# Kernel optimization log

Hardware: AMD Instinct MI355X
Metric: run time of the kernel (lower is better)

Reference implementation:

```python
import jax, jax.numpy as jnp
import numpy as np

D_MODEL = 2048
N_HEADS = 16
HEAD_DIM = D_MODEL // N_HEADS
LN_EPS = 1e-6  # flax.linen.LayerNorm default
NEG_INF = float('-inf')


def _layernorm_scale_only(x, scale):
    # flax LayerNorm with use_bias=False: normalize over last axis, scale only
    mean = jnp.mean(x, axis=-1, keepdims=True)
    var = jnp.var(x, axis=-1, keepdims=True)
    return (x - mean) * jax.lax.rsqrt(var + LN_EPS) * scale


def setup_inputs() -> dict:
    key = jax.random.key(0)
    ks = jax.random.split(key, 4)
    B, S = 2, 2048
    x = jax.random.normal(ks[0], (B, S, D_MODEL), dtype=jnp.float32)
    Wqkv = jax.random.normal(ks[1], (D_MODEL, 3 * D_MODEL), dtype=jnp.float32) * 0.02
    q_ln_scale = jnp.ones((D_MODEL,), dtype=jnp.float32)
    k_ln_scale = jnp.ones((D_MODEL,), dtype=jnp.float32)
    out_W = jax.random.normal(ks[2], (D_MODEL, D_MODEL), dtype=jnp.float32) * 0.02
    return {"x": x, "Wqkv": Wqkv, "q_ln_scale": q_ln_scale,
            "k_ln_scale": k_ln_scale, "out_W": out_W}


def reference(x, Wqkv, q_ln_scale, k_ln_scale, out_W):
    B, S, _ = x.shape
    qkv = jnp.einsum('bsd,de->bse', x, Wqkv)  # [B,S,3*D] (no bias)
    q, k, v = jnp.split(qkv, 3, axis=-1)
    # QK LayerNorm (attn_qk_ln=True, no bias)
    q = _layernorm_scale_only(q, q_ln_scale)
    k = _layernorm_scale_only(k, k_ln_scale)
    # split heads: [B,S,H,Dh]
    q = q.reshape(B, S, N_HEADS, HEAD_DIM)
    k = k.reshape(B, S, N_HEADS, HEAD_DIM)
    v = v.reshape(B, S, N_HEADS, HEAD_DIM)
    # scaled scores [B,H,S,S]
    scores = jnp.einsum('bshd,bthd->bhst', q / jnp.sqrt(jnp.float32(HEAD_DIM)), k)
    # causal mask: triu(ones, k=1) marks strictly-future positions -> -inf
    causal = jnp.triu(jnp.ones((S, S), dtype=bool), 1)
    scores = jnp.where(causal, NEG_INF, scores)
    # kv-cache mask: arange(S) < S - past_position - S = 0 -> all False (no-op
    # with past_position=0 and no layer_past), faithfully omitted.
    attn = jax.nn.softmax(scores, axis=-1)
    ctx = jnp.einsum('bhst,bthd->bshd', attn, v)  # [B,S,H,Dh]
    out = jnp.einsum('bsd,de->bse', ctx.reshape(B, S, D_MODEL), out_W)
    return out
```

## Files before the change

### kernel.cpp

```cpp
#include <hip/hip_runtime.h>


typedef float f32x4 __attribute__((ext_vector_type(4)));
typedef short s16x8 __attribute__((ext_vector_type(8)));
typedef short s16x4 __attribute__((ext_vector_type(4)));

static __device__ __forceinline__ unsigned short f2bf(float f) {
  unsigned u = __builtin_bit_cast(unsigned, f);
  unsigned r = u + 0x7fffu + ((u >> 16) & 1u);
  return (unsigned short)(r >> 16);
}
static __device__ __forceinline__ float bf2f(unsigned short s) {
  unsigned u = ((unsigned)s) << 16;
  return __builtin_bit_cast(float, u);
}

static __device__ __forceinline__ void gload_lds16(const unsigned short* g, unsigned short* l) {
  __builtin_amdgcn_global_load_lds((const __attribute__((address_space(1))) void*)g,
                                   (__attribute__((address_space(3))) void*)l, 16, 0, 0);
}

__global__ __launch_bounds__(256) void k_cvt4(const float4* __restrict__ in,
                                              s16x4* __restrict__ out, int n) {
  int i = blockIdx.x * 256 + threadIdx.x;
  if (i >= n) return;
  float4 v = in[i];
  s16x4 o = { (short)f2bf(v.x), (short)f2bf(v.y), (short)f2bf(v.z), (short)f2bf(v.w) };
  out[i] = o;
}

__global__ __launch_bounds__(256) void k_twT(const float* __restrict__ in,
                                             unsigned short* __restrict__ out,
                                             int K, int N) {
  __shared__ float tile[32][33];
  const int n0 = blockIdx.x * 32, k0 = blockIdx.y * 32;
  const int tx = threadIdx.x & 31, ty = threadIdx.x >> 5;
#pragma unroll
  for (int rr = 0; rr < 4; ++rr) {
    int kr = ty + rr * 8;
    tile[kr][tx] = in[(size_t)(k0 + kr) * N + n0 + tx];
  }
  __syncthreads();
#pragma unroll
  for (int rr = 0; rr < 4; ++rr) {
    int nr = ty + rr * 8;
    out[(size_t)(n0 + nr) * K + k0 + tx] = f2bf(tile[tx][nr]);
  }
}

template <int BF16OUT>
__global__ __launch_bounds__(512, 2) void k_g8p(const unsigned short* __restrict__ A,
                                                const unsigned short* __restrict__ Bt,
                                                void* __restrict__ Cout,
                                                int N, int K, int nbn) {
  __shared__ unsigned short sA[2 * 128 * 64];
  __shared__ unsigned short sB[2 * 2 * 128 * 64];
  const int t = threadIdx.x;
  const int wid = t >> 6, lane = t & 63, g = lane >> 4, l15 = lane & 15;
  const int wm2 = wid >> 2, wn2 = wid & 3;
  const int xr = l15 & 7;

  const int cpx = (int)gridDim.x >> 3;
  const int swz = ((int)blockIdx.x & 7) * cpx + ((int)blockIdx.x >> 3);
  const int m0 = (swz / nbn) * 128, n0 = (swz % nbn) * 256;

  const int srow = t >> 3;
  const int sslot = (t & 7) ^ (srow & 7);
  const unsigned short* pA = A  + (size_t)(m0 + srow) * K + sslot * 8;
  const unsigned short* pB = Bt + (size_t)(n0 + srow) * K + sslot * 8;

  auto stageA = [&](int kt) {
#pragma unroll
    for (int j = 0; j < 2; ++j)
      gload_lds16(pA + (size_t)(j * 64) * K + kt * 64,
                  sA + (kt & 1) * 8192 + j * 4096 + t * 8);
  };
  auto stageB = [&](int kt, int h) {
#pragma unroll
    for (int j = 0; j < 2; ++j)
      gload_lds16(pB + (size_t)(h * 128 + j * 64) * K + kt * 64,
                  sB + (kt & 1) * 16384 + h * 8192 + j * 4096 + t * 8);
  };

  const int sl0 = (g ^ xr) * 8, sl1 = ((4 + g) ^ xr) * 8;
  const int arow = wm2 * 64 + l15;
  const int brow = wn2 * 32 + l15;

  f32x4 acc[2][4][2];
#pragma unroll
  for (int h = 0; h < 2; ++h)
#pragma unroll
    for (int fm = 0; fm < 4; ++fm)
#pragma unroll
      for (int fn = 0; fn < 2; ++fn) acc[h][fm][fn] = (f32x4){0.f, 0.f, 0.f, 0.f};

  const int NK = K >> 6;
  stageA(0); stageB(0, 0); stageB(0, 1);
  asm volatile("s_waitcnt vmcnt(2)" ::: "memory");
  __builtin_amdgcn_sched_barrier(0);
  asm volatile("s_barrier" ::: "memory");

  for (int s = 0; s < NK; ++s) {
    const unsigned short* aT = sA + (s & 1) * 8192;
    const unsigned short* bT = sB + (s & 1) * 16384;
    const bool tail = (s == NK - 1);
    s16x8 af[4][2], bfr[2][2];

#pragma unroll
    for (int fm = 0; fm < 4; ++fm) {
      af[fm][0] = *(const s16x8*)&aT[(arow + fm * 16) * 64 + sl0];
      af[fm][1] = *(const s16x8*)&aT[(arow + fm * 16) * 64 + sl1];
    }
#pragma unroll
    for (int fn = 0; fn < 2; ++fn) {
      bfr[fn][0] = *(const s16x8*)&bT[(brow + fn * 16) * 64 + sl0];
      bfr[fn][1] = *(const s16x8*)&bT[(brow + fn * 16) * 64 + sl1];
    }
    if (!tail) { stageA(s + 1); stageB(s + 1, 0); }
    if (tail) asm volatile("s_waitcnt vmcnt(0)" ::: "memory");
    else      asm volatile("s_waitcnt vmcnt(4)" ::: "memory");
    __builtin_amdgcn_sched_barrier(0);
    asm volatile("s_barrier" ::: "memory");
    __builtin_amdgcn_s_setprio(1);
#pragma unroll
    for (int fm = 0; fm < 4; ++fm)
#pragma unroll
      for (int fn = 0; fn < 2; ++fn)
#pragma unroll
        for (int ks = 0; ks < 2; ++ks)
          acc[0][fm][fn] = __builtin_amdgcn_mfma_f32_16x16x32_bf16(
              af[fm][ks], bfr[fn][ks], acc[0][fm][fn], 0, 0, 0);
    __builtin_amdgcn_s_setprio(0);
    asm volatile("s_barrier" ::: "memory");

#pragma unroll
    for (int fn = 0; fn < 2; ++fn) {
      bfr[fn][0] = *(const s16x8*)&bT[8192 + (brow + fn * 16) * 64 + sl0];
      bfr[fn][1] = *(const s16x8*)&bT[8192 + (brow + fn * 16) * 64 + sl1];
    }
    if (!tail) stageB(s + 1, 1);
    if (tail) asm volatile("s_waitcnt vmcnt(0)" ::: "memory");
    else      asm volatile("s_waitcnt vmcnt(2)" ::: "memory");
    __builtin_amdgcn_sched_barrier(0);
    asm volatile("s_barrier" ::: "memory");
    __builtin_amdgcn_s_setprio(1);
#pragma unroll
    for (int fm = 0; fm < 4; ++fm)
#pragma unroll
      for (int fn = 0; fn < 2; ++fn)
#pragma unroll
        for (int ks = 0; ks < 2; ++ks)
          acc[1][fm][fn] = __builtin_amdgcn_mfma_f32_16x16x32_bf16(
              af[fm][ks], bfr[fn][ks], acc[1][fm][fn], 0, 0, 0);
    __builtin_amdgcn_s_setprio(0);
    asm volatile("s_barrier" ::: "memory");
  }

#pragma unroll
  for (int h = 0; h < 2; ++h)
#pragma unroll
    for (int fm = 0; fm < 4; ++fm)
#pragma unroll
      for (int fn = 0; fn < 2; ++fn)
#pragma unroll
        for (int r = 0; r < 4; ++r) {
          const int row = m0 + wm2 * 64 + fm * 16 + g * 4 + r;
          const int col = n0 + h * 128 + wn2 * 32 + fn * 16 + l15;
          if (BF16OUT)
            ((unsigned short*)Cout)[(size_t)row * N + col] = f2bf(acc[h][fm][fn][r]);
          else
            ((float*)Cout)[(size_t)row * N + col] = acc[h][fm][fn][r];
        }
}

__global__ __launch_bounds__(256) void k_ln(unsigned short* __restrict__ qkv,
                                            const float* __restrict__ qsc,
                                            const float* __restrict__ ksc) {
  __shared__ float red[8];
  const int t = threadIdx.x;
  const int w = t >> 6;
  unsigned short* base = qkv + (size_t)blockIdx.x * 6144;
#pragma unroll
  for (int part = 0; part < 2; ++part) {
    unsigned short* p = base + part * 2048 + t * 8;
    s16x8 v = *(const s16x8*)p;
    float f[8], s = 0.f, q = 0.f;
#pragma unroll
    for (int j = 0; j < 8; j++) { f[j] = bf2f((unsigned short)v[j]); s += f[j]; q += f[j] * f[j]; }
#pragma unroll
    for (int m = 1; m < 64; m <<= 1) { s += __shfl_xor(s, m); q += __shfl_xor(q, m); }
    __syncthreads();
    if ((t & 63) == 0) { red[w] = s; red[4 + w] = q; }
    __syncthreads();
    s = red[0] + red[1] + red[2] + red[3];
    q = red[4] + red[5] + red[6] + red[7];
    float mean = s * (1.f / 2048.f);
    float var = q * (1.f / 2048.f) - mean * mean;
    float inv = rsqrtf(var + 1e-6f);
    const float* sc = part ? ksc : qsc;
    float extra = part ? 1.0f : 0.12751743f;
    s16x8 o;
#pragma unroll
    for (int j = 0; j < 8; j++) o[j] = (short)f2bf((f[j] - mean) * inv * (sc[t * 8 + j] * extra));
    *(s16x8*)p = o;
  }
}

__global__ __launch_bounds__(256) void k_vT(const unsigned short* __restrict__ qkv,
                                            unsigned short* __restrict__ vt) {
  __shared__ unsigned short tl[64][136];
  const int bh = blockIdx.y;
  const int b = bh >> 4, h = bh & 15;
  const int s0 = blockIdx.x * 64;
  const int t = threadIdx.x;
#pragma unroll
  for (int it = 0; it < 4; ++it) {
    int flat = it * 256 + t;
    int r = flat >> 4, c = flat & 15;
    s16x8 v = *(const s16x8*)(qkv + (size_t)(b * 2048 + s0 + r) * 6144 + 4096 + h * 128 + c * 8);
    *((s16x8*)&tl[r][c * 8]) = v;
  }
  __syncthreads();
#pragma unroll
  for (int it = 0; it < 4; ++it) {
    int flat = it * 256 + t;
    int d = flat >> 3, cs = flat & 7;
    s16x8 o;
#pragma unroll
    for (int e = 0; e < 8; e++) {
      int key = (cs >> 2) * 32 + (e >> 2) * 16 + (cs & 3) * 4 + (e & 3);
      o[e] = (short)tl[key][d];
    }
    *(s16x8*)(vt + (size_t)(bh * 128 + d) * 2048 + s0 + cs * 8) = o;
  }
}

__global__ __launch_bounds__(256) void k_attn(const unsigned short* __restrict__ qkv,
                                              const unsigned short* __restrict__ vt,
                                              unsigned short* __restrict__ ctx) {
  __shared__ unsigned short sK[2][64 * 128];
  __shared__ unsigned short sV[2][128 * 64];
  const int t = threadIdx.x;
  const int w = t >> 6, lane = t & 63, g = lane >> 4, l15 = lane & 15;
  const int pair = blockIdx.x, h = blockIdx.y, b = blockIdx.z;
  const int qt0 = 31 - pair, qt1 = pair;
  const int n0 = qt0 + 1;
  const int NT = 33;
  const unsigned short* kbase = qkv + (size_t)(b * 2048) * 6144 + 2048 + h * 128;
  const unsigned short* vbase = vt + (size_t)((b * 16 + h) * 128) * 2048;

  auto issue_kv = [&](int k0, int bufi) {
#pragma unroll
    for (int it2 = 0; it2 < 4; ++it2) {
      int flat = it2 * 256 + t;
      int r = flat >> 4, c = flat & 15;
      gload_lds16(kbase + (size_t)(k0 + r) * 6144 + ((c ^ (r & 15)) * 8),
                  (unsigned short*)&sK[bufi][(it2 * 256 + w * 64) * 8]);
    }
#pragma unroll
    for (int it2 = 0; it2 < 4; ++it2) {
      int flat = it2 * 256 + t;
      int d = flat >> 3, z = flat & 7;
      gload_lds16(vbase + (size_t)d * 2048 + k0 + ((z ^ (d & 7)) * 8),
                  (unsigned short*)&sV[bufi][(it2 * 256 + w * 64) * 8]);
    }
  };

  s16x8 bq[4];
  auto load_q = [&](int q0) {
#pragma unroll
    for (int ks = 0; ks < 4; ++ks)
      bq[ks] = *(const s16x8*)(qkv + (size_t)(b * 2048 + q0 + w * 16 + l15) * 6144 +
                               h * 128 + (ks * 4 + g) * 8);
  };

  f32x4 o[8];
  float mrun, lrun;
  auto reset_state = [&]() {
#pragma unroll
    for (int nd = 0; nd < 8; ++nd) o[nd] = (f32x4){0.f, 0.f, 0.f, 0.f};
    mrun = -INFINITY; lrun = 0.f;
  };
  auto write_o = [&](int q0) {
    float ivr[4];
#pragma unroll
    for (int r = 0; r < 4; ++r) ivr[r] = 1.0f / __shfl(lrun, 4 * g + r);
#pragma unroll
    for (int nd = 0; nd < 8; ++nd) {
      const int col = h * 128 + nd * 16 + l15;
#pragma unroll
      for (int r = 0; r < 4; ++r) {
        const int row = b * 2048 + q0 + w * 16 + 4 * g + r;
        ctx[(size_t)row * 2048 + col] = f2bf(o[nd][r] * ivr[r]);
      }
    }
  };

  reset_state();
  load_q(qt0 * 64);
  issue_kv(0, 0);
  int cur = 0;

  for (int it = 0; it < NT; ++it) {
    const int seg = (it < n0) ? 0 : 1;
    const int qt = seg ? qt1 : qt0;
    const int kt = seg ? it - n0 : it;

    if (it + 1 < NT) {
      const int kn = (it + 1 < n0) ? it + 1 : it + 1 - n0;
      issue_kv(kn * 64, cur ^ 1);
      asm volatile("s_waitcnt vmcnt(8)" ::: "memory");
    } else {
      asm volatile("s_waitcnt vmcnt(0)" ::: "memory");
    }
    __builtin_amdgcn_sched_barrier(0);
    __builtin_amdgcn_s_barrier();

    if (seg == 1 && kt == 0) {
      write_o(qt0 * 64);
      reset_state();
      load_q(qt1 * 64);
    }

    const unsigned short* sKc = &sK[cur][0];
    const unsigned short* sVc = &sV[cur][0];

    f32x4 st[4];
#pragma unroll
    for (int mi = 0; mi < 4; ++mi) st[mi] = (f32x4){0.f, 0.f, 0.f, 0.f};
#pragma unroll
    for (int mi = 0; mi < 4; ++mi) {
#pragma unroll
      for (int ks = 0; ks < 4; ++ks) {
        s16x8 ak = *(const s16x8*)&sKc[(mi * 16 + l15) * 128 + (((ks * 4 + g) ^ l15) * 8)];
        st[mi] = __builtin_amdgcn_mfma_f32_16x16x32_bf16(ak, bq[ks], st[mi], 0, 0, 0);
      }
    }

    if (kt == qt) {
      const int qloc = w * 16 + l15;
#pragma unroll
      for (int mi = 0; mi < 4; ++mi)
#pragma unroll
        for (int r = 0; r < 4; ++r)
          if (mi * 16 + 4 * g + r > qloc) st[mi][r] = -INFINITY;
    }

    float mt = -INFINITY;
#pragma unroll
    for (int mi = 0; mi < 4; ++mi)
#pragma unroll
      for (int r = 0; r < 4; ++r) mt = fmaxf(mt, st[mi][r]);
    mt = fmaxf(mt, __shfl_xor(mt, 16));
    mt = fmaxf(mt, __shfl_xor(mt, 32));

    if (!__all(mt <= mrun + 8.f)) {
      const float mnew = fmaxf(mrun, mt);
      const float alpha = exp2f(mrun - mnew);
      lrun *= alpha;
      float ar[4];
#pragma unroll
      for (int r = 0; r < 4; ++r) ar[r] = __shfl(alpha, 4 * g + r);
#pragma unroll
      for (int nd = 0; nd < 8; ++nd)
#pragma unroll
        for (int r = 0; r < 4; ++r) o[nd][r] *= ar[r];
      mrun = mnew;
    }

    float ls = 0.f;
#pragma unroll
    for (int mi = 0; mi < 4; ++mi)
#pragma unroll
      for (int r = 0; r < 4; ++r) {
        float pp = exp2f(st[mi][r] - mrun);
        st[mi][r] = pp;
        ls += pp;
      }
    ls += __shfl_xor(ls, 16);
    ls += __shfl_xor(ls, 32);
    lrun += ls;

    s16x8 pa01, pa23;
#pragma unroll
    for (int j = 0; j < 8; ++j) {
      pa01[j] = (short)f2bf(st[j >> 2][j & 3]);
      pa23[j] = (short)f2bf(st[2 + (j >> 2)][j & 3]);
    }

#pragma unroll
    for (int nd = 0; nd < 8; ++nd) {
      const int d = nd * 16 + l15;
      const int zs = d & 7;
      s16x8 bv0 = *(const s16x8*)&sVc[d * 64 + ((g ^ zs) * 8)];
      s16x8 bv1 = *(const s16x8*)&sVc[d * 64 + (((4 + g) ^ zs) * 8)];
      o[nd] = __builtin_amdgcn_mfma_f32_16x16x32_bf16(pa01, bv0, o[nd], 0, 0, 0);
      o[nd] = __builtin_amdgcn_mfma_f32_16x16x32_bf16(pa23, bv1, o[nd], 0, 0, 0);
    }

    __builtin_amdgcn_sched_barrier(0);
    __builtin_amdgcn_s_barrier();
    cur ^= 1;
  }
  write_o(qt1 * 64);
}

extern "C" void kernel_launch(void* const* d_in, const int* in_sizes, int n_in,
                              void* d_out, int out_size, void* d_ws, size_t ws_size,
                              hipStream_t stream) {
  (void)in_sizes; (void)n_in; (void)out_size; (void)ws_size;
  const float* x    = (const float*)d_in[0];
  const float* Wqkv = (const float*)d_in[1];
  const float* qsc  = (const float*)d_in[2];
  const float* ksc  = (const float*)d_in[3];
  const float* outW = (const float*)d_in[4];

  char* ws = (char*)d_ws;
  unsigned short* xb  = (unsigned short*)(ws);
  unsigned short* wT  = (unsigned short*)(ws + 16777216);
  unsigned short* owT = (unsigned short*)(ws + 41943040);
  unsigned short* qkv = (unsigned short*)(ws + 50331648);
  unsigned short* vt  = (unsigned short*)(ws + 100663296);
  unsigned short* ctx = xb;

  k_cvt4<<<8192, 256, 0, stream>>>((const float4*)x, (s16x4*)xb, 2097152);
  k_twT<<<dim3(192, 64), 256, 0, stream>>>(Wqkv, wT, 2048, 6144);
  k_twT<<<dim3(64, 64), 256, 0, stream>>>(outW, owT, 2048, 2048);
  k_g8p<1><<<768, 512, 0, stream>>>(xb, wT, qkv, 6144, 2048, 24);
  k_ln<<<4096, 256, 0, stream>>>(qkv, qsc, ksc);
  k_vT<<<dim3(32, 32), 256, 0, stream>>>(qkv, vt);
  k_attn<<<dim3(16, 16, 2), 256, 0, stream>>>(qkv, vt, ctx);
  k_g8p<0><<<256, 512, 0, stream>>>(ctx, owT, d_out, 2048, 2048, 8);
}
```

Before: 280.8 us.

## Use triple-buffered GEMM pipeline with XCD-aware column tile mapping

```diff
diff --git a/kernel.cpp b/kernel.cpp
--- a/kernel.cpp
+++ b/kernel.cpp
@@ -49,37 +49,35 @@
 }
 
 template <int BF16OUT>
-__global__ __launch_bounds__(512, 2) void k_g8p(const unsigned short* __restrict__ A,
+__global__ __launch_bounds__(512, 2) void k_g3b(const unsigned short* __restrict__ A,
                                                 const unsigned short* __restrict__ Bt,
                                                 void* __restrict__ Cout,
-                                                int N, int K, int nbn) {
-  __shared__ unsigned short sA[2 * 128 * 64];
-  __shared__ unsigned short sB[2 * 2 * 128 * 64];
+                                                int N, int K, int npx) {
+  __shared__ unsigned short sA[3 * 128 * 64];
+  __shared__ unsigned short sB[3 * 256 * 64];
   const int t = threadIdx.x;
   const int wid = t >> 6, lane = t & 63, g = lane >> 4, l15 = lane & 15;
   const int wm2 = wid >> 2, wn2 = wid & 3;
   const int xr = l15 & 7;
 
-  const int cpx = (int)gridDim.x >> 3;
-  const int swz = ((int)blockIdx.x & 7) * cpx + ((int)blockIdx.x >> 3);
-  const int m0 = (swz / nbn) * 128, n0 = (swz % nbn) * 256;
+  const int xcd = (int)blockIdx.x & 7, idx = (int)blockIdx.x >> 3;
+  const int m0 = (idx / npx) * 128;
+  const int n0 = (xcd * npx + idx % npx) * 256;
 
   const int srow = t >> 3;
   const int sslot = (t & 7) ^ (srow & 7);
   const unsigned short* pA = A  + (size_t)(m0 + srow) * K + sslot * 8;
   const unsigned short* pB = Bt + (size_t)(n0 + srow) * K + sslot * 8;
 
-  auto stageA = [&](int kt) {
+  auto stage = [&](int kt, int buf) {
 #pragma unroll
     for (int j = 0; j < 2; ++j)
       gload_lds16(pA + (size_t)(j * 64) * K + kt * 64,
-                  sA + (kt & 1) * 8192 + j * 4096 + t * 8);
-  };
-  auto stageB = [&](int kt, int h) {
-#pragma unroll
-    for (int j = 0; j < 2; ++j)
-      gload_lds16(pB + (size_t)(h * 128 + j * 64) * K + kt * 64,
-                  sB + (kt & 1) * 16384 + h * 8192 + j * 4096 + t * 8);
+                  sA + buf * 8192 + j * 4096 + t * 8);
+#pragma unroll
+    for (int j = 0; j < 4; ++j)
+      gload_lds16(pB + (size_t)(j * 64) * K + kt * 64,
+                  sB + buf * 16384 + j * 4096 + t * 8);
   };
 
   const int sl0 = (g ^ xr) * 8, sl1 = ((4 + g) ^ xr) * 8;
@@ -95,65 +93,53 @@
       for (int fn = 0; fn < 2; ++fn) acc[h][fm][fn] = (f32x4){0.f, 0.f, 0.f, 0.f};
 
   const int NK = K >> 6;
-  stageA(0); stageB(0, 0); stageB(0, 1);
-  asm volatile("s_waitcnt vmcnt(2)" ::: "memory");
-  __builtin_amdgcn_sched_barrier(0);
-  asm volatile("s_barrier" ::: "memory");
+  stage(0, 0);
+  stage(1, 1);
+  int b0 = 0, b1 = 1, b2 = 2;
 
   for (int s = 0; s < NK; ++s) {
-    const unsigned short* aT = sA + (s & 1) * 8192;
-    const unsigned short* bT = sB + (s & 1) * 16384;
-    const bool tail = (s == NK - 1);
-    s16x8 af[4][2], bfr[2][2];
-
+    if (s + 2 < NK) stage(s + 2, b2);
+
+    if (s + 2 < NK)      asm volatile("s_waitcnt vmcnt(12)" ::: "memory");
+    else if (s + 1 < NK) asm volatile("s_waitcnt vmcnt(6)" ::: "memory");
+    else                 asm volatile("s_waitcnt vmcnt(0)" ::: "memory");
+    __builtin_amdgcn_sched_barrier(0);
+    __builtin_amdgcn_s_barrier();
+    __builtin_amdgcn_sched_barrier(0);
+
+    const unsigned short* aT = sA + b0 * 8192;
+    const unsigned short* bT = sB + b0 * 16384;
+    s16x8 af[4][2], bfr[2][2][2];
 #pragma unroll
     for (int fm = 0; fm < 4; ++fm) {
       af[fm][0] = *(const s16x8*)&aT[(arow + fm * 16) * 64 + sl0];
       af[fm][1] = *(const s16x8*)&aT[(arow + fm * 16) * 64 + sl1];
     }
 #pragma unroll
-    for (int fn = 0; fn < 2; ++fn) {
-      bfr[fn][0] = *(const s16x8*)&bT[(brow + fn * 16) * 64 + sl0];
-      bfr[fn][1] = *(const s16x8*)&bT[(brow + fn * 16) * 64 + sl1];
-    }
-    if (!tail) { stageA(s + 1); stageB(s + 1, 0); }
-    if (tail) asm volatile("s_waitcnt vmcnt(0)" ::: "memory");
-    else      asm volatile("s_waitcnt vmcnt(4)" ::: "memory");
+    for (int h = 0; h < 2; ++h)
+#pragma unroll
+      for (int fn = 0; fn < 2; ++fn) {
+        bfr[h][fn][0] = *(const s16x8*)&bT[(h * 128 + brow + fn * 16) * 64 + sl0];
+        bfr[h][fn][1] = *(const s16x8*)&bT[(h * 128 + brow + fn * 16) * 64 + sl1];
+      }
+
+    __builtin_amdgcn_s_setprio(1);
+#pragma unroll
+    for (int fm = 0; fm < 4; ++fm)
+#pragma unroll
+      for (int h = 0; h < 2; ++h)
+#pragma unroll
+        for (int fn = 0; fn < 2; ++fn)
+#pragma unroll
+          for (int ks = 0; ks < 2; ++ks)
+            acc[h][fm][fn] = __builtin_amdgcn_mfma_f32_16x16x32_bf16(
+                af[fm][ks], bfr[h][fn][ks], acc[h][fm][fn], 0, 0, 0);
+    __builtin_amdgcn_s_setprio(0);
+
     __builtin_amdgcn_sched_barrier(0);
-    asm volatile("s_barrier" ::: "memory");
-    __builtin_amdgcn_s_setprio(1);
-#pragma unroll
-    for (int fm = 0; fm < 4; ++fm)
-#pragma unroll
-      for (int fn = 0; fn < 2; ++fn)
-#pragma unroll
-        for (int ks = 0; ks < 2; ++ks)
-          acc[0][fm][fn] = __builtin_amdgcn_mfma_f32_16x16x32_bf16(
-              af[fm][ks], bfr[fn][ks], acc[0][fm][fn], 0, 0, 0);
-    __builtin_amdgcn_s_setprio(0);
-    asm volatile("s_barrier" ::: "memory");
-
-#pragma unroll
-    for (int fn = 0; fn < 2; ++fn) {
-      bfr[fn][0] = *(const s16x8*)&bT[8192 + (brow + fn * 16) * 64 + sl0];
-      bfr[fn][1] = *(const s16x8*)&bT[8192 + (brow + fn * 16) * 64 + sl1];
-    }
-    if (!tail) stageB(s + 1, 1);
-    if (tail) asm volatile("s_waitcnt vmcnt(0)" ::: "memory");
-    else      asm volatile("s_waitcnt vmcnt(2)" ::: "memory");
-    __builtin_amdgcn_sched_barrier(0);
-    asm volatile("s_barrier" ::: "memory");
-    __builtin_amdgcn_s_setprio(1);
-#pragma unroll
-    for (int fm = 0; fm < 4; ++fm)
-#pragma unroll
-      for (int fn = 0; fn < 2; ++fn)
-#pragma unroll
-        for (int ks = 0; ks < 2; ++ks)
-          acc[1][fm][fn] = __builtin_amdgcn_mfma_f32_16x16x32_bf16(
-              af[fm][ks], bfr[fn][ks], acc[1][fm][fn], 0, 0, 0);
-    __builtin_amdgcn_s_setprio(0);
-    asm volatile("s_barrier" ::: "memory");
+    __builtin_amdgcn_s_barrier();
+
+    int tmp = b0; b0 = b1; b1 = b2; b2 = tmp;
   }
 
 #pragma unroll
@@ -426,9 +412,9 @@
   k_cvt4<<<8192, 256, 0, stream>>>((const float4*)x, (s16x4*)xb, 2097152);
   k_twT<<<dim3(192, 64), 256, 0, stream>>>(Wqkv, wT, 2048, 6144);
   k_twT<<<dim3(64, 64), 256, 0, stream>>>(outW, owT, 2048, 2048);
-  k_g8p<1><<<768, 512, 0, stream>>>(xb, wT, qkv, 6144, 2048, 24);
+  k_g3b<1><<<768, 512, 0, stream>>>(xb, wT, qkv, 6144, 2048, 3);
   k_ln<<<4096, 256, 0, stream>>>(qkv, qsc, ksc);
   k_vT<<<dim3(32, 32), 256, 0, stream>>>(qkv, vt);
   k_attn<<<dim3(16, 16, 2), 256, 0, stream>>>(qkv, vt, ctx);
-  k_g8p<0><<<256, 512, 0, stream>>>(ctx, owT, d_out, 2048, 2048, 8);
-}
+  k_g3b<0><<<256, 512, 0, stream>>>(ctx, owT, d_out, 2048, 2048, 1);
+}
```

Measured after the change: 306.5 us. +9.1%, slower.

## Triple-buffer GEMM LDS stages and map column tiles per XCD

Applied to the files above, without the earlier changes.

```diff
diff --git a/kernel.cpp b/kernel.cpp
--- a/kernel.cpp
+++ b/kernel.cpp
@@ -49,37 +49,43 @@
 }
 
 template <int BF16OUT>
-__global__ __launch_bounds__(512, 2) void k_g8p(const unsigned short* __restrict__ A,
+__global__ __launch_bounds__(512, 2) void k_gp3(const unsigned short* __restrict__ A,
                                                 const unsigned short* __restrict__ Bt,
                                                 void* __restrict__ Cout,
-                                                int N, int K, int nbn) {
-  __shared__ unsigned short sA[2 * 128 * 64];
-  __shared__ unsigned short sB[2 * 2 * 128 * 64];
+                                                int N, int K, int npx) {
+  __shared__ unsigned short sA[3 * 128 * 64];
+  __shared__ unsigned short sB[3 * 256 * 64];
   const int t = threadIdx.x;
   const int wid = t >> 6, lane = t & 63, g = lane >> 4, l15 = lane & 15;
   const int wm2 = wid >> 2, wn2 = wid & 3;
   const int xr = l15 & 7;
 
-  const int cpx = (int)gridDim.x >> 3;
-  const int swz = ((int)blockIdx.x & 7) * cpx + ((int)blockIdx.x >> 3);
-  const int m0 = (swz / nbn) * 128, n0 = (swz % nbn) * 256;
+  const int xcd = (int)blockIdx.x & 7, idx = (int)blockIdx.x >> 3;
+  const int m0 = (idx / npx) * 128;
+  const int n0 = (xcd * npx + idx % npx) * 256;
 
   const int srow = t >> 3;
   const int sslot = (t & 7) ^ (srow & 7);
   const unsigned short* pA = A  + (size_t)(m0 + srow) * K + sslot * 8;
   const unsigned short* pB = Bt + (size_t)(n0 + srow) * K + sslot * 8;
 
-  auto stageA = [&](int kt) {
+  auto stageA = [&](int kt, int buf) {
 #pragma unroll
     for (int j = 0; j < 2; ++j)
       gload_lds16(pA + (size_t)(j * 64) * K + kt * 64,
-                  sA + (kt & 1) * 8192 + j * 4096 + t * 8);
-  };
-  auto stageB = [&](int kt, int h) {
+                  sA + buf * 8192 + j * 4096 + t * 8);
+  };
+  auto stageB0 = [&](int kt, int buf) {
 #pragma unroll
     for (int j = 0; j < 2; ++j)
-      gload_lds16(pB + (size_t)(h * 128 + j * 64) * K + kt * 64,
-                  sB + (kt & 1) * 16384 + h * 8192 + j * 4096 + t * 8);
+      gload_lds16(pB + (size_t)(j * 64) * K + kt * 64,
+                  sB + buf * 16384 + j * 4096 + t * 8);
+  };
+  auto stageB1 = [&](int kt, int buf) {
+#pragma unroll
+    for (int j = 0; j < 2; ++j)
+      gload_lds16(pB + (size_t)(128 + j * 64) * K + kt * 64,
+                  sB + buf * 16384 + 8192 + j * 4096 + t * 8);
   };
 
   const int sl0 = (g ^ xr) * 8, sl1 = ((4 + g) ^ xr) * 8;
@@ -95,15 +101,17 @@
       for (int fn = 0; fn < 2; ++fn) acc[h][fm][fn] = (f32x4){0.f, 0.f, 0.f, 0.f};
 
   const int NK = K >> 6;
-  stageA(0); stageB(0, 0); stageB(0, 1);
-  asm volatile("s_waitcnt vmcnt(2)" ::: "memory");
+  stageA(0, 0); stageB0(0, 0); stageB1(0, 0);
+  stageA(1, 1); stageB0(1, 1); stageB1(1, 1);
+  asm volatile("s_waitcnt vmcnt(8)" ::: "memory");
   __builtin_amdgcn_sched_barrier(0);
   asm volatile("s_barrier" ::: "memory");
-
+  __builtin_amdgcn_sched_barrier(0);
+
+  int b0 = 0, b2 = 2;
   for (int s = 0; s < NK; ++s) {
-    const unsigned short* aT = sA + (s & 1) * 8192;
-    const unsigned short* bT = sB + (s & 1) * 16384;
-    const bool tail = (s == NK - 1);
+    const unsigned short* aT = sA + b0 * 8192;
+    const unsigned short* bT = sB + b0 * 16384;
     s16x8 af[4][2], bfr[2][2];
 
 #pragma unroll
@@ -116,11 +124,13 @@
       bfr[fn][0] = *(const s16x8*)&bT[(brow + fn * 16) * 64 + sl0];
       bfr[fn][1] = *(const s16x8*)&bT[(brow + fn * 16) * 64 + sl1];
     }
-    if (!tail) { stageA(s + 1); stageB(s + 1, 0); }
-    if (tail) asm volatile("s_waitcnt vmcnt(0)" ::: "memory");
-    else      asm volatile("s_waitcnt vmcnt(4)" ::: "memory");
+    if (s + 2 < NK) { stageA(s + 2, b2); stageB0(s + 2, b2); }
+    if (s + 2 < NK)       asm volatile("s_waitcnt vmcnt(10)" ::: "memory");
+    else if (s == NK - 2) asm volatile("s_waitcnt vmcnt(6)"  ::: "memory");
+    else                  asm volatile("s_waitcnt vmcnt(0)"  ::: "memory");
     __builtin_amdgcn_sched_barrier(0);
     asm volatile("s_barrier" ::: "memory");
+    __builtin_amdgcn_sched_barrier(0);
     __builtin_amdgcn_s_setprio(1);
 #pragma unroll
     for (int fm = 0; fm < 4; ++fm)
@@ -131,6 +141,7 @@
           acc[0][fm][fn] = __builtin_amdgcn_mfma_f32_16x16x32_bf16(
               af[fm][ks], bfr[fn][ks], acc[0][fm][fn], 0, 0, 0);
     __builtin_amdgcn_s_setprio(0);
+    __builtin_amdgcn_sched_barrier(0);
     asm volatile("s_barrier" ::: "memory");
 
 #pragma unroll
@@ -138,11 +149,12 @@
       bfr[fn][0] = *(const s16x8*)&bT[8192 + (brow + fn * 16) * 64 + sl0];
       bfr[fn][1] = *(const s16x8*)&bT[8192 + (brow + fn * 16) * 64 + sl1];
     }
-    if (!tail) stageB(s + 1, 1);
-    if (tail) asm volatile("s_waitcnt vmcnt(0)" ::: "memory");
-    else      asm volatile("s_waitcnt vmcnt(2)" ::: "memory");
+    if (s + 2 < NK) stageB1(s + 2, b2);
+    if (s + 2 < NK)       asm volatile("s_waitcnt vmcnt(8)" ::: "memory");
+    else if (s == NK - 2) asm volatile("s_waitcnt vmcnt(2)" ::: "memory");
     __builtin_amdgcn_sched_barrier(0);
     asm volatile("s_barrier" ::: "memory");
+    __builtin_amdgcn_sched_barrier(0);
     __builtin_amdgcn_s_setprio(1);
 #pragma unroll
     for (int fm = 0; fm < 4; ++fm)
@@ -153,7 +165,11 @@
           acc[1][fm][fn] = __builtin_amdgcn_mfma_f32_16x16x32_bf16(
               af[fm][ks], bfr[fn][ks], acc[1][fm][fn], 0, 0, 0);
     __builtin_amdgcn_s_setprio(0);
+    __builtin_amdgcn_sched_barrier(0);
     asm volatile("s_barrier" ::: "memory");
+
+    b0 = (b0 == 2) ? 0 : b0 + 1;
+    b2 = (b2 == 2) ? 0 : b2 + 1;
   }
 
 #pragma unroll
@@ -426,9 +442,9 @@
   k_cvt4<<<8192, 256, 0, stream>>>((const float4*)x, (s16x4*)xb, 2097152);
   k_twT<<<dim3(192, 64), 256, 0, stream>>>(Wqkv, wT, 2048, 6144);
   k_twT<<<dim3(64, 64), 256, 0, stream>>>(outW, owT, 2048, 2048);
-  k_g8p<1><<<768, 512, 0, stream>>>(xb, wT, qkv, 6144, 2048, 24);
+  k_gp3<1><<<768, 512, 0, stream>>>(xb, wT, qkv, 6144, 2048, 3);
   k_ln<<<4096, 256, 0, stream>>>(qkv, qsc, ksc);
   k_vT<<<dim3(32, 32), 256, 0, stream>>>(qkv, vt);
   k_attn<<<dim3(16, 16, 2), 256, 0, stream>>>(qkv, vt, ctx);
-  k_g8p<0><<<256, 512, 0, stream>>>(ctx, owT, d_out, 2048, 2048, 8);
-}
+  k_gp3<0><<<256, 512, 0, stream>>>(ctx, owT, d_out, 2048, 2048, 1);
+}
```

After: 288.3 us. 2.7% more time.
